# Performance work log

Measured on AMD Instinct MI355X. Metric: run time of the kernel, lower is better.

The kernel has to match this reference:

```python
import math
import jax, jax.numpy as jnp
import numpy as np

D_HEAD = 64


def setup_inputs() -> dict:
    key = jax.random.key(0)
    ks = jax.random.split(key, 8)
    B, S, D, H, Dh = 2, 2048, 1024, 16, D_HEAD
    return {
        "x": jax.random.normal(ks[0], (B, S, D), dtype=jnp.float32),
        "attention_mask": jnp.ones((B, S), dtype=bool),
        "query_weight": jax.random.normal(ks[1], (H, D, Dh), dtype=jnp.float32),
        "query_bias": jax.random.normal(ks[2], (H, Dh), dtype=jnp.float32),
        "key_weight": jax.random.normal(ks[3], (H, D, Dh), dtype=jnp.float32),
        "key_bias": jax.random.normal(ks[4], (H, Dh), dtype=jnp.float32),
        "value_weight": jax.random.normal(ks[5], (H, D, Dh), dtype=jnp.float32),
        "value_bias": jax.random.normal(ks[6], (H, Dh), dtype=jnp.float32),
        "output_weight": jax.random.normal(ks[7], (D, D), dtype=jnp.float32),
    }


def reference(x, attention_mask, query_weight, query_bias, key_weight, key_bias,
              value_weight, value_bias, output_weight):
    B, S, D = x.shape
    H, _, Dh = query_weight.shape
    # per-head projections: [B, S, H, Dh]
    q = jnp.einsum('bsd,hde->bshe', x, query_weight) + query_bias
    k = jnp.einsum('bsd,hde->bshe', x, key_weight) + key_bias
    v = jnp.einsum('bsd,hde->bshe', x, value_weight) + value_bias
    # scores: [B, H, Sq, Sk]
    scores = jnp.einsum('bqhe,bkhe->bhqk', q, k)
    # additive mask: subtract inf where mask is False (original: score -= where(mask,0,inf))
    neg = jnp.where(attention_mask, 0.0, jnp.inf)[:, None, None, :]
    scores = scores - neg
    probs = jax.nn.softmax(scores / math.sqrt(Dh), axis=3)
    attn = jnp.einsum('bhqk,bkhe->bhqe', probs, v)
    attn = jnp.transpose(attn, (0, 2, 1, 3)).reshape(B, S, H * Dh)
    return jnp.einsum('bsd,de->bse', attn, output_weight)
```

## Files before the change

### kernel.cpp

```cpp
#include <hip/hip_runtime.h>
#include <math.h>

#define BATCH 2
#define SEQ 2048
#define DMODEL 1024
#define NH 16
#define DH 64

typedef short s16x8 __attribute__((ext_vector_type(8)));
typedef float f32x4 __attribute__((ext_vector_type(4)));

__device__ __forceinline__ ushort f2bf(float x) {
    unsigned u = __float_as_uint(x);
    u += 0x7FFFu + ((u >> 16) & 1u);
    return (ushort)(u >> 16);
}
__device__ __forceinline__ float bf2f(ushort h) {
    return __uint_as_float(((unsigned)h) << 16);
}

__global__ __launch_bounds__(256) void transpose_qkv_w(
    const float* __restrict__ wq, const float* __restrict__ wk,
    const float* __restrict__ wv,
    ushort* __restrict__ qThi, ushort* __restrict__ qTlo,
    ushort* __restrict__ kThi, ushort* __restrict__ kTlo,
    ushort* __restrict__ vT)
{
    const int z = blockIdx.z;
    const int which = z >> 4, hh = z & 15;
    const float* src = (which == 0) ? wq : (which == 1) ? wk : wv;
    ushort* dhi = (which == 0) ? qThi : (which == 1) ? kThi : vT;
    ushort* dlo = (which == 0) ? qTlo : (which == 1) ? kTlo : vT;
    const int split = (which < 2);

    const size_t zoff = (size_t)hh * DMODEL * DH;
    const int r0 = blockIdx.y * 64;
    __shared__ float T[64][68];
    const int t = threadIdx.x;
    #pragma unroll
    for (int p = 0; p < 4; ++p) {
        const int slot = t + 256 * p;
        const int row = slot >> 4, ch = (slot & 15) * 4;
        *(float4*)&T[row][ch] =
            *(const float4*)&src[zoff + (size_t)(r0 + row) * DH + ch];
    }
    __syncthreads();
    const int e = t >> 2, dch = (t & 3) * 16;
    s16x8 h0, h1, l0, l1;
    #pragma unroll
    for (int j = 0; j < 8; ++j) {
        const float v = T[dch + j][e];
        const ushort hi = f2bf(v);
        h0[j] = (short)hi; l0[j] = (short)f2bf(v - bf2f(hi));
    }
    #pragma unroll
    for (int j = 0; j < 8; ++j) {
        const float v = T[dch + 8 + j][e];
        const ushort hi = f2bf(v);
        h1[j] = (short)hi; l1[j] = (short)f2bf(v - bf2f(hi));
    }
    const size_t ob = zoff + (size_t)e * DMODEL + r0 + dch;
    *(s16x8*)&dhi[ob]     = h0;
    *(s16x8*)&dhi[ob + 8] = h1;
    if (split) {
        *(s16x8*)&dlo[ob]     = l0;
        *(s16x8*)&dlo[ob + 8] = l1;
    }
}

__global__ __launch_bounds__(256) void transpose_wo(
    const float* __restrict__ src, ushort* __restrict__ dhi)
{
    const int r0 = blockIdx.y * 64, c0 = blockIdx.x * 64;
    __shared__ float T[64][68];
    const int t = threadIdx.x;
    #pragma unroll
    for (int p = 0; p < 4; ++p) {
        const int slot = t + 256 * p;
        const int row = slot >> 4, ch = (slot & 15) * 4;
        *(float4*)&T[row][ch] =
            *(const float4*)&src[(size_t)(r0 + row) * DMODEL + c0 + ch];
    }
    __syncthreads();
    const int e = t >> 2, dch = (t & 3) * 16;
    s16x8 h0, h1;
    #pragma unroll
    for (int j = 0; j < 8; ++j) h0[j] = (short)f2bf(T[dch + j][e]);
    #pragma unroll
    for (int j = 0; j < 8; ++j) h1[j] = (short)f2bf(T[dch + 8 + j][e]);
    const size_t ob = (size_t)(c0 + e) * DMODEL + r0 + dch;
    *(s16x8*)&dhi[ob]     = h0;
    *(s16x8*)&dhi[ob + 8] = h1;
}

__global__ __launch_bounds__(256) void qkv_fused(
    const float* __restrict__ x,
    const ushort* __restrict__ wqThi, const ushort* __restrict__ wqTlo,
    const ushort* __restrict__ wkThi, const ushort* __restrict__ wkTlo,
    const ushort* __restrict__ wvT,
    const float* __restrict__ bq, const float* __restrict__ bk,
    const float* __restrict__ bv,
    ushort* __restrict__ qhi, ushort* __restrict__ qlo,
    ushort* __restrict__ khi, ushort* __restrict__ klo,
    ushort* __restrict__ vT)
{
    const int h = blockIdx.x;
    const int m0 = blockIdx.y * 64;
    const size_t whoff = (size_t)h * DH * DMODEL;

    __shared__ ushort Ah[64 * 32];
    __shared__ ushort Al[64 * 32];
    __shared__ ushort Bqh[64 * 32];
    __shared__ ushort Bql[64 * 32];
    __shared__ ushort Bkh[64 * 32];
    __shared__ ushort Bkl[64 * 32];
    __shared__ ushort Bv [64 * 32];

    const int t = threadIdx.x;
    const int w = t >> 6, g = (t >> 4) & 3, i = t & 15;

    f32x4 aq[4] = {}, ak[4] = {}, av_[4] = {};

    float4 xa[2];
    s16x8 wq8h, wq8l, wk8h, wk8l, wv8;

    const int xrow = t >> 2;
    const int xch  = (t & 3) * 8;
    const int wrow = t >> 2;
    const int wch  = (t & 3) * 8;
    const size_t wbase = whoff + (size_t)wrow * DMODEL + wch;

    const int xcs = xch ^ (((xrow >> 1) & 3) * 8);
    const int wcs = wch ^ (((wrow >> 1) & 3) * 8);
    const int fcs = (g * 8) ^ (((i >> 1) & 3) * 8);

    #define QKV_LOAD(K0)                                                      \
        xa[0] = *(const float4*)&x[(size_t)(m0 + xrow) * DMODEL + (K0) + xch];     \
        xa[1] = *(const float4*)&x[(size_t)(m0 + xrow) * DMODEL + (K0) + xch + 4]; \
        wq8h = *(const s16x8*)&wqThi[wbase + (K0)];                           \
        wq8l = *(const s16x8*)&wqTlo[wbase + (K0)];                           \
        wk8h = *(const s16x8*)&wkThi[wbase + (K0)];                           \
        wk8l = *(const s16x8*)&wkTlo[wbase + (K0)];                           \
        wv8  = *(const s16x8*)&wvT[wbase + (K0)];

    QKV_LOAD(0)

    for (int k0 = 0; k0 < DMODEL; k0 += 32) {
        __syncthreads();

        {
            const float vv[8] = {xa[0].x, xa[0].y, xa[0].z, xa[0].w,
                                 xa[1].x, xa[1].y, xa[1].z, xa[1].w};
            s16x8 h8, l8;
            #pragma unroll
            for (int j = 0; j < 8; ++j) {
                const ushort hi = f2bf(vv[j]);
                h8[j] = (short)hi;
                l8[j] = (short)f2bf(vv[j] - bf2f(hi));
            }
            *(s16x8*)&Ah[xrow * 32 + xcs] = h8;
            *(s16x8*)&Al[xrow * 32 + xcs] = l8;
        }
        *(s16x8*)&Bqh[wrow * 32 + wcs] = wq8h;
        *(s16x8*)&Bql[wrow * 32 + wcs] = wq8l;
        *(s16x8*)&Bkh[wrow * 32 + wcs] = wk8h;
        *(s16x8*)&Bkl[wrow * 32 + wcs] = wk8l;
        *(s16x8*)&Bv [wrow * 32 + wcs] = wv8;

        if (k0 + 32 < DMODEL) {
            QKV_LOAD(k0 + 32)
        }
        __syncthreads();

        const int ar = w * 16 + i;
        const s16x8 ah = *(const s16x8*)&Ah[ar * 32 + fcs];
        const s16x8 al = *(const s16x8*)&Al[ar * 32 + fcs];
        #pragma unroll
        for (int nb = 0; nb < 4; ++nb) {
            const int br = nb * 16 + i;
            const s16x8 bqh8 = *(const s16x8*)&Bqh[br * 32 + fcs];
            const s16x8 bql8 = *(const s16x8*)&Bql[br * 32 + fcs];
            const s16x8 bkh8 = *(const s16x8*)&Bkh[br * 32 + fcs];
            const s16x8 bkl8 = *(const s16x8*)&Bkl[br * 32 + fcs];
            const s16x8 bv8  = *(const s16x8*)&Bv [br * 32 + fcs];
            aq[nb] = __builtin_amdgcn_mfma_f32_16x16x32_bf16(ah, bqh8, aq[nb], 0, 0, 0);
            aq[nb] = __builtin_amdgcn_mfma_f32_16x16x32_bf16(al, bqh8, aq[nb], 0, 0, 0);
            aq[nb] = __builtin_amdgcn_mfma_f32_16x16x32_bf16(ah, bql8, aq[nb], 0, 0, 0);
            ak[nb] = __builtin_amdgcn_mfma_f32_16x16x32_bf16(ah, bkh8, ak[nb], 0, 0, 0);
            ak[nb] = __builtin_amdgcn_mfma_f32_16x16x32_bf16(al, bkh8, ak[nb], 0, 0, 0);
            ak[nb] = __builtin_amdgcn_mfma_f32_16x16x32_bf16(ah, bkl8, ak[nb], 0, 0, 0);
            av_[nb] = __builtin_amdgcn_mfma_f32_16x16x32_bf16(ah, bv8, av_[nb], 0, 0, 0);
        }
    }
    #undef QKV_LOAD

    const int b = m0 >> 11;
    const int sloc0 = (m0 & 2047) + w * 16 + g * 4;
    const size_t bh_base = (size_t)(b * NH + h);

    #pragma unroll
    for (int nb = 0; nb < 4; ++nb) {
        const float bia = bq[h * DH + nb * 16 + i];
        #pragma unroll
        for (int r = 0; r < 4; ++r) {
            const float val = (aq[nb][r] + bia) * 0.125f;
            const ushort hi = f2bf(val);
            const size_t idx = (bh_base * SEQ + sloc0 + r) * DH + nb * 16 + i;
            qhi[idx] = hi;
            qlo[idx] = f2bf(val - bf2f(hi));
        }
    }
    #pragma unroll
    for (int nb = 0; nb < 4; ++nb) {
        const float bia = bk[h * DH + nb * 16 + i];
        #pragma unroll
        for (int r = 0; r < 4; ++r) {
            const float val = ak[nb][r] + bia;
            const ushort hi = f2bf(val);
            const size_t idx = (bh_base * SEQ + sloc0 + r) * DH + nb * 16 + i;
            khi[idx] = hi;
            klo[idx] = f2bf(val - bf2f(hi));
        }
    }
    #pragma unroll
    for (int nb = 0; nb < 4; ++nb) {
        const float bia = bv[h * DH + nb * 16 + i];
        ushort4 pk; ushort* pp = (ushort*)&pk;
        #pragma unroll
        for (int r = 0; r < 4; ++r)
            pp[r] = f2bf(av_[nb][r] + bia);
        *(ushort4*)&vT[(bh_base * DH + nb * 16 + i) * SEQ + sloc0] = pk;
    }
}

__global__ __launch_bounds__(256) void flash4(
    const ushort* __restrict__ qhi, const ushort* __restrict__ qlo,
    const ushort* __restrict__ khi, const ushort* __restrict__ klo,
    const ushort* __restrict__ vT, ushort* __restrict__ attn2)
{
    const int bid = blockIdx.x;
    const int id2 = (bid & 7) * 64 + (bid >> 3);
    const int bh = id2 >> 4, qblk = id2 & 15;
    const int bi = bh >> 4, h = bh & 15;
    const int s0 = qblk * 128;

    __shared__ ushort Kh[64 * 72];
    __shared__ ushort Kl[64 * 72];
    __shared__ ushort Vt[64 * 72];

    const int t = threadIdx.x;
    const int w = t >> 6, g = (t >> 4) & 3, i = t & 15;

    s16x8 qh[2][2], ql[2][2];
    #pragma unroll
    for (int grp = 0; grp < 2; ++grp) {
        const size_t qb = ((size_t)bh * SEQ + s0 + w * 32 + grp * 16 + i) * DH;
        #pragma unroll
        for (int sl = 0; sl < 2; ++sl) {
            qh[grp][sl] = *(const s16x8*)&qhi[qb + sl * 32 + g * 8];
            ql[grp][sl] = *(const s16x8*)&qlo[qb + sl * 32 + g * 8];
        }
    }

    int krow[4];
    #pragma unroll
    for (int cb = 0; cb < 4; ++cb) {
        const int gp = i >> 2, r = i & 3;
        const int bb = cb >> 1, hh = cb & 1;
        const int gg = hh ? (gp ^ 2) : gp;
        krow[cb] = 32 * bb + 8 * gg + 4 * hh + r;
    }

    f32x4 acc[2][4] = {};
    float m_i[2] = {-INFINITY, -INFINITY}, l_i[2] = {0.f, 0.f};

    const size_t kbase = (size_t)bh * SEQ * DH;
    const size_t vbase = (size_t)bh * DH * SEQ;

    s16x8 ckh[2], ckl[2], cvt[2];
    #pragma unroll
    for (int p = 0; p < 2; ++p) {
        const int slot = t + 256 * p;
        const int row = slot >> 3, ch = (slot & 7) * 8;
        ckh[p] = *(const s16x8*)&khi[kbase + (size_t)row * DH + ch];
        ckl[p] = *(const s16x8*)&klo[kbase + (size_t)row * DH + ch];
        cvt[p] = *(const s16x8*)&vT[vbase + (size_t)row * SEQ + ch];
    }

    for (int kt = 0; kt < SEQ / 64; ++kt) {
        __syncthreads();
        #pragma unroll
        for (int p = 0; p < 2; ++p) {
            const int slot = t + 256 * p;
            const int row = slot >> 3, ch = (slot & 7) * 8;
            *(s16x8*)&Kh[row * 72 + ch] = ckh[p];
            *(s16x8*)&Kl[row * 72 + ch] = ckl[p];
            *(s16x8*)&Vt[row * 72 + ch] = cvt[p];
        }
        if (kt + 1 < SEQ / 64) {
            #pragma unroll
            for (int p = 0; p < 2; ++p) {
                const int slot = t + 256 * p;
                const int row = slot >> 3, ch = (slot & 7) * 8;
                ckh[p] = *(const s16x8*)&khi[kbase + (size_t)((kt + 1) * 64 + row) * DH + ch];
                ckl[p] = *(const s16x8*)&klo[kbase + (size_t)((kt + 1) * 64 + row) * DH + ch];
                cvt[p] = *(const s16x8*)&vT[vbase + (size_t)row * SEQ + (kt + 1) * 64 + ch];
            }
        }
        __syncthreads();

        f32x4 st[2][4] = {};
        __builtin_amdgcn_s_setprio(1);
        #pragma unroll
        for (int cb = 0; cb < 4; ++cb) {
            #pragma unroll
            for (int sl = 0; sl < 2; ++sl) {
                const int off = krow[cb] * 72 + sl * 32 + g * 8;
                const s16x8 kh = *(const s16x8*)&Kh[off];
                const s16x8 kl = *(const s16x8*)&Kl[off];
                #pragma unroll
                for (int grp = 0; grp < 2; ++grp) {
                    st[grp][cb] = __builtin_amdgcn_mfma_f32_16x16x32_bf16(kh, qh[grp][sl], st[grp][cb], 0, 0, 0);
                    st[grp][cb] = __builtin_amdgcn_mfma_f32_16x16x32_bf16(kh, ql[grp][sl], st[grp][cb], 0, 0, 0);
                    st[grp][cb] = __builtin_amdgcn_mfma_f32_16x16x32_bf16(kl, qh[grp][sl], st[grp][cb], 0, 0, 0);
                }
            }
        }
        __builtin_amdgcn_s_setprio(0);

        s16x8 pa0[2], pa1[2];
        #pragma unroll
        for (int grp = 0; grp < 2; ++grp) {
            float mloc = -INFINITY;
            #pragma unroll
            for (int cb = 0; cb < 4; ++cb)
                #pragma unroll
                for (int r = 0; r < 4; ++r) mloc = fmaxf(mloc, st[grp][cb][r]);
            mloc = fmaxf(mloc, __shfl_xor(mloc, 16));
            mloc = fmaxf(mloc, __shfl_xor(mloc, 32));
            const float m_new = fmaxf(m_i[grp], mloc);
            const float resc = __expf(m_i[grp] - m_new);
            float sum = 0.f;
            #pragma unroll
            for (int cb = 0; cb < 4; ++cb)
                #pragma unroll
                for (int r = 0; r < 4; ++r) {
                    const float pv = __expf(st[grp][cb][r] - m_new);
                    st[grp][cb][r] = pv; sum += pv;
                }
            sum += __shfl_xor(sum, 16);
            sum += __shfl_xor(sum, 32);
            m_i[grp] = m_new;
            l_i[grp] = l_i[grp] * resc + sum;

            unsigned pk[8];
            #pragma unroll
            for (int cb = 0; cb < 4; ++cb) {
                asm volatile("v_cvt_pk_bf16_f32 %0, %1, %2"
                             : "=v"(pk[cb * 2]) : "v"(st[grp][cb][0]), "v"(st[grp][cb][1]));
                asm volatile("v_cvt_pk_bf16_f32 %0, %1, %2"
                             : "=v"(pk[cb * 2 + 1]) : "v"(st[grp][cb][2]), "v"(st[grp][cb][3]));
            }
            asm volatile("v_permlane32_swap_b32 %0, %1" : "+v"(pk[2]), "+v"(pk[3]));
            asm volatile("v_permlane32_swap_b32 %0, %1" : "+v"(pk[3]), "+v"(pk[2]));
            asm volatile("v_permlane32_swap_b32 %0, %1" : "+v"(pk[6]), "+v"(pk[7]));
            asm volatile("v_permlane32_swap_b32 %0, %1" : "+v"(pk[7]), "+v"(pk[6]));
            union { s16x8 v; unsigned u[4]; } a0, a1;
            a0.u[0] = pk[0]; a0.u[1] = pk[1]; a0.u[2] = pk[3]; a0.u[3] = pk[2];
            a1.u[0] = pk[4]; a1.u[1] = pk[5]; a1.u[2] = pk[7]; a1.u[3] = pk[6];
            pa0[grp] = a0.v; pa1[grp] = a1.v;

            #pragma unroll
            for (int r = 0; r < 4; ++r) {
                const float rq = __shfl(resc, g * 4 + r);
                #pragma unroll
                for (int nb = 0; nb < 4; ++nb) acc[grp][nb][r] *= rq;
            }
        }

        __builtin_amdgcn_s_setprio(1);
        #pragma unroll
        for (int b = 0; b < 2; ++b) {
            #pragma unroll
            for (int nb = 0; nb < 4; ++nb) {
                const s16x8 vf = *(const s16x8*)&Vt[(nb * 16 + i) * 72 + b * 32 + g * 8];
                acc[0][nb] = __builtin_amdgcn_mfma_f32_16x16x32_bf16(
                    b ? pa1[0] : pa0[0], vf, acc[0][nb], 0, 0, 0);
                acc[1][nb] = __builtin_amdgcn_mfma_f32_16x16x32_bf16(
                    b ? pa1[1] : pa0[1], vf, acc[1][nb], 0, 0, 0);
            }
        }
        __builtin_amdgcn_s_setprio(0);
    }

    #pragma unroll
    for (int grp = 0; grp < 2; ++grp)
        #pragma unroll
        for (int r = 0; r < 4; ++r) {
            const float lq = __shfl(l_i[grp], g * 4 + r);
            const float inv = 1.0f / lq;
            const int srow = s0 + w * 32 + grp * 16 + g * 4 + r;
            ushort* orow = attn2 + ((size_t)bi * SEQ + srow) * DMODEL + h * DH;
            #pragma unroll
            for (int nb = 0; nb < 4; ++nb)
                orow[nb * 16 + i] = f2bf(acc[grp][nb][r] * inv);
        }
}

__global__ __launch_bounds__(256) void out_mfma(
    const ushort* __restrict__ a, const ushort* __restrict__ woT,
    float* __restrict__ out)
{
    const int n0 = blockIdx.x * 64;
    const int m0 = blockIdx.y * 64;
    __shared__ ushort As[64 * 72];
    __shared__ ushort Bs[64 * 72];
    const int t = threadIdx.x;
    const int w = t >> 6, g = (t >> 4) & 3, i = t & 15;

    f32x4 acc[4] = {};
    s16x8 a8[2], b8[2];

    #define OUT_LOAD(K0)                                                      \
        _Pragma("unroll")                                                     \
        for (int p = 0; p < 2; ++p) {                                         \
            const int slot = t + 256 * p;                                     \
            a8[p] = *(const s16x8*)&a[(size_t)(m0 + (slot >> 3)) * DMODEL + (K0) + (slot & 7) * 8]; \
        }                                                                     \
        _Pragma("unroll")                                                     \
        for (int p = 0; p < 2; ++p) {                                         \
            const int slot = t + 256 * p;                                     \
            b8[p] = *(const s16x8*)&woT[(size_t)(n0 + (slot >> 3)) * DMODEL + (K0) + (slot & 7) * 8]; \
        }

    OUT_LOAD(0)

    for (int k0 = 0; k0 < DMODEL; k0 += 64) {
        __syncthreads();
        #pragma unroll
        for (int p = 0; p < 2; ++p) {
            const int slot = t + 256 * p;
            *(s16x8*)&As[(slot >> 3) * 72 + (slot & 7) * 8] = a8[p];
        }
        #pragma unroll
        for (int p = 0; p < 2; ++p) {
            const int slot = t + 256 * p;
            *(s16x8*)&Bs[(slot >> 3) * 72 + (slot & 7) * 8] = b8[p];
        }
        if (k0 + 64 < DMODEL) {
            OUT_LOAD(k0 + 64)
        }
        __syncthreads();

        #pragma unroll
        for (int sl = 0; sl < 2; ++sl) {
            const s16x8 af = *(const s16x8*)&As[(w * 16 + i) * 72 + sl * 32 + g * 8];
            #pragma unroll
            for (int nb = 0; nb < 4; ++nb) {
                const s16x8 bf8 = *(const s16x8*)&Bs[(nb * 16 + i) * 72 + sl * 32 + g * 8];
                acc[nb] = __builtin_amdgcn_mfma_f32_16x16x32_bf16(af, bf8, acc[nb], 0, 0, 0);
            }
        }
    }
    #undef OUT_LOAD

    #pragma unroll
    for (int nb = 0; nb < 4; ++nb)
        #pragma unroll
        for (int r = 0; r < 4; ++r)
            out[(size_t)(m0 + w * 16 + g * 4 + r) * DMODEL + n0 + nb * 16 + i] =
                acc[nb][r];
}

extern "C" void kernel_launch(void* const* d_in, const int* in_sizes, int n_in,
                              void* d_out, int out_size, void* d_ws, size_t ws_size,
                              hipStream_t stream) {
    const float* x  = (const float*)d_in[0];
    const float* wq = (const float*)d_in[2];
    const float* bq = (const float*)d_in[3];
    const float* wk = (const float*)d_in[4];
    const float* bk = (const float*)d_in[5];
    const float* wv = (const float*)d_in[6];
    const float* bv = (const float*)d_in[7];
    const float* wo = (const float*)d_in[8];
    float* out = (float*)d_out;

    char* ws = (char*)d_ws;
    ushort* wqThi = (ushort*)(ws + 0);
    ushort* wqTlo = (ushort*)(ws + 2097152);
    ushort* wkThi = (ushort*)(ws + 4194304);
    ushort* wkTlo = (ushort*)(ws + 6291456);
    ushort* wvT   = (ushort*)(ws + 8388608);
    ushort* woT   = (ushort*)(ws + 10485760);
    ushort* qhi   = (ushort*)(ws + 12582912);
    ushort* qlo   = (ushort*)(ws + 20971520);
    ushort* khi   = (ushort*)(ws + 29360128);
    ushort* klo   = (ushort*)(ws + 37748736);
    ushort* vTb   = (ushort*)(ws + 46137344);
    ushort* attn2 = (ushort*)(ws + 54525952);

    transpose_qkv_w<<<dim3(1, 16, 48), 256, 0, stream>>>(
        wq, wk, wv, wqThi, wqTlo, wkThi, wkTlo, wvT);
    transpose_wo<<<dim3(16, 16), 256, 0, stream>>>(wo, woT);

    qkv_fused<<<dim3(16, 64), 256, 0, stream>>>(x, wqThi, wqTlo, wkThi, wkTlo, wvT,
                                                bq, bk, bv, qhi, qlo, khi, klo, vTb);
    flash4<<<dim3(512), 256, 0, stream>>>(qhi, qlo, khi, klo, vTb, attn2);
    out_mfma<<<dim3(16, 64), 256, 0, stream>>>(attn2, woT, out);
}
```

Baseline: 200.5 us.

## Use exp2 softmax with lazy rescale and reorganize QKV MFMA tiling

The Q scale now folds in log2(e), so the flash kernel can use the hardware exp2 instruction instead of __expf. It also skips the running-max rescale unless the block max grows by more than 8, and computes the row max with three-input max ops. Separately, the QKV projection kernel swaps which operand each wave keeps in registers: B fragments are loaded once and A fragments are iterated. The output writes change to match, with Q and K stores merged into one loop. The intent is to cut transcendental and VALU work in the softmax and reduce LDS reads in the projection. The lazy rescale lets probabilities reach up to 2^8 before renormalising, which loosens bf16 accuracy somewhat.

```diff
diff --git a/kernel.cpp b/kernel.cpp
--- a/kernel.cpp
+++ b/kernel.cpp
@@ -17,6 +17,9 @@
 }
 __device__ __forceinline__ float bf2f(ushort h) {
     return __uint_as_float(((unsigned)h) << 16);
+}
+__device__ __forceinline__ float fm3(float a, float b, float c) {
+    return fmaxf(fmaxf(a, b), c);
 }
 
 __global__ __launch_bounds__(256) void transpose_qkv_w(
@@ -172,68 +175,64 @@
         }
         __syncthreads();
 
-        const int ar = w * 16 + i;
-        const s16x8 ah = *(const s16x8*)&Ah[ar * 32 + fcs];
-        const s16x8 al = *(const s16x8*)&Al[ar * 32 + fcs];
-        #pragma unroll
-        for (int nb = 0; nb < 4; ++nb) {
-            const int br = nb * 16 + i;
-            const s16x8 bqh8 = *(const s16x8*)&Bqh[br * 32 + fcs];
-            const s16x8 bql8 = *(const s16x8*)&Bql[br * 32 + fcs];
-            const s16x8 bkh8 = *(const s16x8*)&Bkh[br * 32 + fcs];
-            const s16x8 bkl8 = *(const s16x8*)&Bkl[br * 32 + fcs];
-            const s16x8 bv8  = *(const s16x8*)&Bv [br * 32 + fcs];
-            aq[nb] = __builtin_amdgcn_mfma_f32_16x16x32_bf16(ah, bqh8, aq[nb], 0, 0, 0);
-            aq[nb] = __builtin_amdgcn_mfma_f32_16x16x32_bf16(al, bqh8, aq[nb], 0, 0, 0);
-            aq[nb] = __builtin_amdgcn_mfma_f32_16x16x32_bf16(ah, bql8, aq[nb], 0, 0, 0);
-            ak[nb] = __builtin_amdgcn_mfma_f32_16x16x32_bf16(ah, bkh8, ak[nb], 0, 0, 0);
-            ak[nb] = __builtin_amdgcn_mfma_f32_16x16x32_bf16(al, bkh8, ak[nb], 0, 0, 0);
-            ak[nb] = __builtin_amdgcn_mfma_f32_16x16x32_bf16(ah, bkl8, ak[nb], 0, 0, 0);
-            av_[nb] = __builtin_amdgcn_mfma_f32_16x16x32_bf16(ah, bv8, av_[nb], 0, 0, 0);
+        const int br = w * 16 + i;
+        const s16x8 bqh8 = *(const s16x8*)&Bqh[br * 32 + fcs];
+        const s16x8 bql8 = *(const s16x8*)&Bql[br * 32 + fcs];
+        const s16x8 bkh8 = *(const s16x8*)&Bkh[br * 32 + fcs];
+        const s16x8 bkl8 = *(const s16x8*)&Bkl[br * 32 + fcs];
+        const s16x8 bv8  = *(const s16x8*)&Bv [br * 32 + fcs];
+        #pragma unroll
+        for (int rf = 0; rf < 4; ++rf) {
+            const int ar = rf * 16 + i;
+            const s16x8 ah = *(const s16x8*)&Ah[ar * 32 + fcs];
+            const s16x8 al = *(const s16x8*)&Al[ar * 32 + fcs];
+            aq[rf] = __builtin_amdgcn_mfma_f32_16x16x32_bf16(ah, bqh8, aq[rf], 0, 0, 0);
+            aq[rf] = __builtin_amdgcn_mfma_f32_16x16x32_bf16(al, bqh8, aq[rf], 0, 0, 0);
+            aq[rf] = __builtin_amdgcn_mfma_f32_16x16x32_bf16(ah, bql8, aq[rf], 0, 0, 0);
+            ak[rf] = __builtin_amdgcn_mfma_f32_16x16x32_bf16(ah, bkh8, ak[rf], 0, 0, 0);
+            ak[rf] = __builtin_amdgcn_mfma_f32_16x16x32_bf16(al, bkh8, ak[rf], 0, 0, 0);
+            ak[rf] = __builtin_amdgcn_mfma_f32_16x16x32_bf16(ah, bkl8, ak[rf], 0, 0, 0);
+            av_[rf] = __builtin_amdgcn_mfma_f32_16x16x32_bf16(ah, bv8, av_[rf], 0, 0, 0);
         }
     }
     #undef QKV_LOAD
 
     const int b = m0 >> 11;
-    const int sloc0 = (m0 & 2047) + w * 16 + g * 4;
+    const int col = w * 16 + i;
+    const int sbase = (m0 & 2047) + g * 4;
     const size_t bh_base = (size_t)(b * NH + h);
 
-    #pragma unroll
-    for (int nb = 0; nb < 4; ++nb) {
-        const float bia = bq[h * DH + nb * 16 + i];
+    const float QSCALE = 0.125f * 1.44269504088896f;
+    #pragma unroll
+    for (int rf = 0; rf < 4; ++rf) {
+        const float biaq = bq[h * DH + col];
+        const float biak = bk[h * DH + col];
         #pragma unroll
         for (int r = 0; r < 4; ++r) {
-            const float val = (aq[nb][r] + bia) * 0.125f;
-            const ushort hi = f2bf(val);
-            const size_t idx = (bh_base * SEQ + sloc0 + r) * DH + nb * 16 + i;
-            qhi[idx] = hi;
-            qlo[idx] = f2bf(val - bf2f(hi));
-        }
-    }
-    #pragma unroll
-    for (int nb = 0; nb < 4; ++nb) {
-        const float bia = bk[h * DH + nb * 16 + i];
-        #pragma unroll
-        for (int r = 0; r < 4; ++r) {
-            const float val = ak[nb][r] + bia;
-            const ushort hi = f2bf(val);
-            const size_t idx = (bh_base * SEQ + sloc0 + r) * DH + nb * 16 + i;
-            khi[idx] = hi;
-            klo[idx] = f2bf(val - bf2f(hi));
-        }
-    }
-    #pragma unroll
-    for (int nb = 0; nb < 4; ++nb) {
-        const float bia = bv[h * DH + nb * 16 + i];
+            const int sloc = sbase + rf * 16 + r;
+            const size_t idx = (bh_base * SEQ + sloc) * DH + col;
+            const float vq = (aq[rf][r] + biaq) * QSCALE;
+            const ushort hq = f2bf(vq);
+            qhi[idx] = hq;
+            qlo[idx] = f2bf(vq - bf2f(hq));
+            const float vk = ak[rf][r] + biak;
+            const ushort hk = f2bf(vk);
+            khi[idx] = hk;
+            klo[idx] = f2bf(vk - bf2f(hk));
+        }
+    }
+    #pragma unroll
+    for (int rf = 0; rf < 4; ++rf) {
+        const float bia = bv[h * DH + col];
         ushort4 pk; ushort* pp = (ushort*)&pk;
         #pragma unroll
         for (int r = 0; r < 4; ++r)
-            pp[r] = f2bf(av_[nb][r] + bia);
-        *(ushort4*)&vT[(bh_base * DH + nb * 16 + i) * SEQ + sloc0] = pk;
-    }
-}
-
-__global__ __launch_bounds__(256) void flash4(
+            pp[r] = f2bf(av_[rf][r] + bia);
+        *(ushort4*)&vT[(bh_base * DH + col) * SEQ + sbase + rf * 16] = pk;
+    }
+}
+
+__global__ __launch_bounds__(256) void flash5(
     const ushort* __restrict__ qhi, const ushort* __restrict__ qlo,
     const ushort* __restrict__ khi, const ushort* __restrict__ klo,
     const ushort* __restrict__ vT, ushort* __restrict__ attn2)
@@ -331,27 +330,39 @@
         s16x8 pa0[2], pa1[2];
         #pragma unroll
         for (int grp = 0; grp < 2; ++grp) {
-            float mloc = -INFINITY;
-            #pragma unroll
-            for (int cb = 0; cb < 4; ++cb)
-                #pragma unroll
-                for (int r = 0; r < 4; ++r) mloc = fmaxf(mloc, st[grp][cb][r]);
+            float t0 = fm3(st[grp][0][0], st[grp][0][1], st[grp][0][2]);
+            float t1 = fm3(st[grp][0][3], st[grp][1][0], st[grp][1][1]);
+            float t2 = fm3(st[grp][1][2], st[grp][1][3], st[grp][2][0]);
+            float t3 = fm3(st[grp][2][1], st[grp][2][2], st[grp][2][3]);
+            float t4 = fm3(st[grp][3][0], st[grp][3][1], st[grp][3][2]);
+            float mloc = fmaxf(fm3(t0, t1, t2), fm3(t3, t4, st[grp][3][3]));
             mloc = fmaxf(mloc, __shfl_xor(mloc, 16));
             mloc = fmaxf(mloc, __shfl_xor(mloc, 32));
-            const float m_new = fmaxf(m_i[grp], mloc);
-            const float resc = __expf(m_i[grp] - m_new);
+
+            if (!__all(mloc - m_i[grp] <= 8.0f)) {
+                const float m_new = fmaxf(m_i[grp], mloc);
+                const float resc = __builtin_amdgcn_exp2f(m_i[grp] - m_new);
+                m_i[grp] = m_new;
+                l_i[grp] *= resc;
+                #pragma unroll
+                for (int r = 0; r < 4; ++r) {
+                    const float rq = __shfl(resc, g * 4 + r);
+                    #pragma unroll
+                    for (int nb = 0; nb < 4; ++nb) acc[grp][nb][r] *= rq;
+                }
+            }
+
             float sum = 0.f;
             #pragma unroll
             for (int cb = 0; cb < 4; ++cb)
                 #pragma unroll
                 for (int r = 0; r < 4; ++r) {
-                    const float pv = __expf(st[grp][cb][r] - m_new);
+                    const float pv = __builtin_amdgcn_exp2f(st[grp][cb][r] - m_i[grp]);
                     st[grp][cb][r] = pv; sum += pv;
                 }
             sum += __shfl_xor(sum, 16);
             sum += __shfl_xor(sum, 32);
-            m_i[grp] = m_new;
-            l_i[grp] = l_i[grp] * resc + sum;
+            l_i[grp] += sum;
 
             unsigned pk[8];
             #pragma unroll
@@ -369,13 +380,6 @@
             a0.u[0] = pk[0]; a0.u[1] = pk[1]; a0.u[2] = pk[3]; a0.u[3] = pk[2];
             a1.u[0] = pk[4]; a1.u[1] = pk[5]; a1.u[2] = pk[7]; a1.u[3] = pk[6];
             pa0[grp] = a0.v; pa1[grp] = a1.v;
-
-            #pragma unroll
-            for (int r = 0; r < 4; ++r) {
-                const float rq = __shfl(resc, g * 4 + r);
-                #pragma unroll
-                for (int nb = 0; nb < 4; ++nb) acc[grp][nb][r] *= rq;
-            }
         }
 
         __builtin_amdgcn_s_setprio(1);
@@ -505,6 +509,6 @@
 
     qkv_fused<<<dim3(16, 64), 256, 0, stream>>>(x, wqThi, wqTlo, wkThi, wkTlo, wvT,
                                                 bq, bk, bv, qhi, qlo, khi, klo, vTb);
-    flash4<<<dim3(512), 256, 0, stream>>>(qhi, qlo, khi, klo, vTb, attn2);
+    flash5<<<dim3(512), 256, 0, stream>>>(qhi, qlo, khi, klo, vTb, attn2);
     out_mfma<<<dim3(16, 64), 256, 0, stream>>>(attn2, woT, out);
 }
```

Result: no change. 196.6 us, median of 3 (-1.9%).
